# Kernel optimization log

Hardware: AMD Instinct MI355X
Metric: run time of the kernel (lower is better)

Reference implementation:

```python
import jax, jax.numpy as jnp
import numpy as np

N = 50000      # nodes
E = 800000     # edges
FEAT = 128     # input feature dim
EMB = 256      # embed_dim = heads * hid
H = 4          # attention heads
C = 64         # hid_dim per head
PED = 32       # positional encoding dim
NEG_SLOPE = 0.2


def setup_inputs() -> dict:
    key = jax.random.key(0)
    ks = jax.random.split(key, 20)
    s = lambda i, shape, sc=0.1: jax.random.normal(ks[i], shape, jnp.float32) * sc
    return {
        "x": s(0, (N, FEAT), 1.0),
        "x_masked": s(1, (N, FEAT), 1.0),
        "PE": s(2, (N, PED), 1.0),
        "PE_noise": s(3, (N, PED), 1.0),
        "edge_index": jax.random.randint(ks[4], (2, E), 0, N),
        # PEG positional encoder (linear + relu)
        "W_peg": s(5, (PED, PED)), "b_peg": jnp.zeros((PED,), jnp.float32),
        # GAT layer 0
        "W0": s(6, (FEAT, H * C)), "a_s0": s(7, (H, C)), "a_d0": s(8, (H, C)),
        "w_pe0": s(9, (H,)), "W_u0": s(10, (PED, PED)),
        # GAT layer 1
        "W1": s(11, (EMB, H * C)), "a_s1": s(12, (H, C)), "a_d1": s(13, (H, C)),
        "w_pe1": s(14, (H,)), "W_u1": s(15, (PED, PED)),
    }


def _gat(x, pe, src, dst, W, a_s, a_d, w_pe, W_u):
    # PE-aware GATConv: standard GAT attention + PE-distance bias per head.
    xp = (x @ W).reshape(-1, H, C)                       # [N,H,C]
    al_s = (xp * a_s).sum(-1)                            # [N,H]
    al_d = (xp * a_d).sum(-1)                            # [N,H]
    dist = jnp.sqrt(((pe[src] - pe[dst]) ** 2).sum(-1) + 1e-8)   # [E]
    logits = jax.nn.leaky_relu(al_s[src] + al_d[dst], NEG_SLOPE) \
             + dist[:, None] * w_pe                      # [E,H]
    # segment softmax over incoming edges of each dst node
    m = jax.ops.segment_max(logits, dst, num_segments=N)
    e = jnp.exp(logits - m[dst])
    den = jax.ops.segment_sum(e, dst, num_segments=N)
    alpha = e / (den[dst] + 1e-16)                       # [E,H]
    out = jax.ops.segment_sum(alpha[:, :, None] * xp[src], dst,
                              num_segments=N).reshape(-1, H * C)  # [N,H*C]
    pe_out = jax.nn.relu(pe @ W_u)                       # per-layer PE update
    return out, pe_out


def reference(x, x_masked, PE, PE_noise, W_peg, b_peg,
              W0, a_s0, a_d0, w_pe0, W_u0,
              W1, a_s1, a_d1, w_pe1, W_u1, edge_index):
    src, dst = edge_index[0], edge_index[1]
    # PEG encoder on both PE branches
    pe = jax.nn.relu(PE @ W_peg + b_peg)
    pe_n = jax.nn.relu(PE_noise @ W_peg + b_peg)
    # layer 0 (dual branches; eval mode -> dropout is identity)
    h, pe_n = _gat(x, pe_n, src, dst, W0, a_s0, a_d0, w_pe0, W_u0)
    hm, pe = _gat(x_masked, pe, src, dst, W0, a_s0, a_d0, w_pe0, W_u0)
    h = jax.nn.relu(h)
    hm = jax.nn.relu(hm)
    # layer 1 (last layer: no activation)
    h, pe_n = _gat(h, pe_n, src, dst, W1, a_s1, a_d1, w_pe1, W_u1)
    hm, pe = _gat(hm, pe, src, dst, W1, a_s1, a_d1, w_pe1, W_u1)
    return (hm, pe_n)
```

## Files before the change

### kernel.cpp

```cpp
#include <hip/hip_runtime.h>
#include <hip/hip_bf16.h>

#define N_NODES 50000
#define N_EDGES 800000
#define NEG_SLOPE 0.2f

typedef __hip_bfloat16 bf16;
typedef __attribute__((ext_vector_type(8))) short short8;
typedef __attribute__((ext_vector_type(4))) float f32x4;
typedef __attribute__((ext_vector_type(2))) float f32x2;

__device__ __forceinline__ float b2f(bf16 x) { return __bfloat162float(x); }

__device__ __forceinline__ float ldsel(const void* p, size_t i, int isbf) {
  return isbf ? __bfloat162float(((const bf16*)p)[i]) : ((const float*)p)[i];
}
__device__ __forceinline__ void stsel(void* p, size_t i, int isbf, float v) {
  if (isbf) ((bf16*)p)[i] = __float2bfloat16(v);
  else ((float*)p)[i] = v;
}

__device__ __forceinline__ int block_detect(const unsigned short* __restrict__ probe) {
  __shared__ int wcount;
  int tid = threadIdx.x;
  if (tid == 0) wcount = 0;
  __syncthreads();
  int ex = (probe[2 * tid] >> 7) & 0xFF;
  unsigned long long m = __ballot(ex >= 0x85);
  if ((tid & 63) == 0) atomicAdd(&wcount, __popcll(m));
  __syncthreads();
  return wcount < 8;
}

struct CvtJobs {
  const void* src[10];
  float* dst[10];
  int n[10];
};
__global__ __launch_bounds__(256) void prep_kernel(CvtJobs jobs,
                                                   const unsigned short* __restrict__ probe,
                                                   const void* __restrict__ W0in,
                                                   bf16* __restrict__ Wt0,
                                                   const void* __restrict__ W1in,
                                                   bf16* __restrict__ Wt1,
                                                   int* __restrict__ flag) {
  int tid = threadIdx.x;
  int isbf = block_detect(probe);
  int b = blockIdx.x;
  if (b == 0 && tid == 0) *flag = isbf;
  if (b < 16) {
    for (int j = 0; j < 10; j++) {
      int n = jobs.n[j];
      const void* s = jobs.src[j];
      float* d = jobs.dst[j];
      for (int i = b * 256 + tid; i < n; i += 16 * 256) d[i] = ldsel(s, i, isbf);
    }
  } else if (b < 16 + 128) {
    int i = (b - 16) * 256 + tid;
    int n = i >> 7, k = i & 127;
    Wt0[i] = __float2bfloat16(ldsel(W0in, (size_t)k * 256 + n, isbf));
  } else {
    int i = (b - 144) * 256 + tid;
    int n = i >> 8, k = i & 255;
    Wt1[i] = __float2bfloat16(ldsel(W1in, (size_t)k * 256 + n, isbf));
  }
}

__global__ __launch_bounds__(256) void peg_all(const void* __restrict__ pen,
                                               const void* __restrict__ pem,
                                               const float* __restrict__ Wpeg,
                                               const float* __restrict__ bpeg,
                                               const float* __restrict__ Wu0,
                                               const float* __restrict__ Wu1,
                                               void* out, size_t out_off,
                                               char* __restrict__ blob0,
                                               char* __restrict__ blob1,
                                               const int* __restrict__ flag) {
  __shared__ float w1[1024], w2[1024], w3[1024];
  __shared__ float rowA[256], rowB[256];
  int isbf = *flag;
  int tid = threadIdx.x;
  int b = blockIdx.x;
  bool c3 = b < (N_NODES / 8);
  int n0 = (c3 ? b : b - N_NODES / 8) * 8;
  const void* in = c3 ? pen : pem;
  for (int i = tid; i < 1024; i += 256) {
    w1[i] = Wpeg[i];
    w2[i] = Wu0[i];
    if (c3) w3[i] = Wu1[i];
  }
  rowA[tid] = ldsel(in, (size_t)n0 * 32 + tid, isbf);
  __syncthreads();
  int col = tid & 31, ln = tid >> 5;
  size_t bi = ((size_t)(n0 + ln)) * 64 + col;
  float acc = bpeg[col];
#pragma unroll
  for (int j = 0; j < 32; j++) acc += rowA[ln * 32 + j] * w1[j * 32 + col];
  acc = fmaxf(acc, 0.f);
  if (!c3) ((bf16*)blob0)[bi] = __float2bfloat16(acc);
  rowB[tid] = acc;
  __syncthreads();
  acc = 0.f;
#pragma unroll
  for (int j = 0; j < 32; j++) acc += rowB[ln * 32 + j] * w2[j * 32 + col];
  acc = fmaxf(acc, 0.f);
  if (!c3) {
    ((bf16*)blob1)[bi] = __float2bfloat16(acc);
    return;
  }
  rowA[tid] = acc;
  __syncthreads();
  acc = 0.f;
#pragma unroll
  for (int j = 0; j < 32; j++) acc += rowA[ln * 32 + j] * w3[j * 32 + col];
  stsel(out, out_off + (size_t)n0 * 32 + tid, isbf, fmaxf(acc, 0.f));
}

template <int K, bool A_DUAL>
__global__ __launch_bounds__(256) void mfma_gemm(const void* __restrict__ Ap,
                                                 const bf16* __restrict__ Bt,
                                                 bf16* __restrict__ C, int M,
                                                 const float* __restrict__ a_sf,
                                                 const float* __restrict__ a_df,
                                                 char* __restrict__ blob,
                                                 float* __restrict__ al_d,
                                                 const int* __restrict__ flag) {
  constexpr int LDK = 136;
  __shared__ short a_lds[64 * LDK];
  __shared__ short b_lds[64 * LDK];
  __shared__ float lds_al[128];
  int nrt = (M + 63) / 64;
  int bid = blockIdx.x;
  int xcd = bid & 7;
  int jj = bid >> 3;
  int col_t = jj & 3;
  int row_t = (jj >> 2) * 8 + xcd;
  if (row_t >= nrt) return;
  int isbf = A_DUAL ? *flag : 1;
  int tid = threadIdx.x;
  int row0 = row_t * 64;
  int col0 = col_t * 64;
  int lane = tid & 63;
  int wv = tid >> 6;
  int wm = (wv & 1) * 32, wn = (wv >> 1) * 32;
  int l15 = lane & 15, quad = lane >> 4;
  if (tid < 128) lds_al[tid] = 0.f;
  f32x4 acc00 = {0.f, 0.f, 0.f, 0.f}, acc01 = acc00, acc10 = acc00, acc11 = acc00;

  for (int kb = 0; kb < K; kb += 128) {
    if (kb) __syncthreads();
    for (int idx = tid; idx < 64 * 16; idx += 256) {
      int r = idx >> 4, sidx = idx & 15;
      int gr = row0 + r;
      size_t gi = (size_t)gr * K + kb + sidx * 8;
      uint4 av = make_uint4(0u, 0u, 0u, 0u);
      if (A_DUAL && !isbf) {
        if (gr < M) {
          float4 f0 = ((const float4*)Ap)[gi / 4];
          float4 f1 = ((const float4*)Ap)[gi / 4 + 1];
          union { uint4 v; bf16 h[8]; } o;
          o.h[0] = __float2bfloat16(f0.x);
          o.h[1] = __float2bfloat16(f0.y);
          o.h[2] = __float2bfloat16(f0.z);
          o.h[3] = __float2bfloat16(f0.w);
          o.h[4] = __float2bfloat16(f1.x);
          o.h[5] = __float2bfloat16(f1.y);
          o.h[6] = __float2bfloat16(f1.z);
          o.h[7] = __float2bfloat16(f1.w);
          av = o.v;
        }
      } else {
        if (gr < M) av = *(const uint4*)&((const bf16*)Ap)[gi];
      }
      *(uint4*)&a_lds[r * LDK + sidx * 8] = av;
      *(uint4*)&b_lds[r * LDK + sidx * 8] =
          *(const uint4*)&Bt[(size_t)(col0 + r) * K + kb + sidx * 8];
    }
    __syncthreads();
#pragma unroll
    for (int k0 = 0; k0 < 128; k0 += 32) {
      int ko = k0 + quad * 8;
      short8 a0 = *(const short8*)&a_lds[(wm + l15) * LDK + ko];
      short8 a1 = *(const short8*)&a_lds[(wm + 16 + l15) * LDK + ko];
      short8 b0 = *(const short8*)&b_lds[(wn + l15) * LDK + ko];
      short8 b1 = *(const short8*)&b_lds[(wn + 16 + l15) * LDK + ko];
      acc00 = __builtin_amdgcn_mfma_f32_16x16x32_bf16(a0, b0, acc00, 0, 0, 0);
      acc01 = __builtin_amdgcn_mfma_f32_16x16x32_bf16(a0, b1, acc01, 0, 0, 0);
      acc10 = __builtin_amdgcn_mfma_f32_16x16x32_bf16(a1, b0, acc10, 0, 0, 0);
      acc11 = __builtin_amdgcn_mfma_f32_16x16x32_bf16(a1, b1, acc11, 0, 0, 0);
    }
  }
  const f32x4* accs[2][2] = {{&acc00, &acc01}, {&acc10, &acc11}};
  float as0 = a_sf[col0 + wn + l15], as1 = a_sf[col0 + wn + 16 + l15];
  float ad0 = a_df[col0 + wn + l15], ad1 = a_df[col0 + wn + 16 + l15];
#pragma unroll
  for (int i = 0; i < 2; i++) {
    float sp[4], dp[4];
#pragma unroll
    for (int r = 0; r < 4; r++) {
      float v0 = (*accs[i][0])[r], v1 = (*accs[i][1])[r];
      sp[r] = v0 * as0 + v1 * as1;
      dp[r] = v0 * ad0 + v1 * ad1;
      int grow = row0 + wm + i * 16 + quad * 4 + r;
      if (grow < M) {
        C[(size_t)grow * 256 + col0 + wn + l15] = __float2bfloat16(v0);
        C[(size_t)grow * 256 + col0 + wn + 16 + l15] = __float2bfloat16(v1);
      }
    }
#pragma unroll
    for (int off = 1; off < 16; off <<= 1) {
#pragma unroll
      for (int r = 0; r < 4; r++) {
        sp[r] += __shfl_xor(sp[r], off);
        dp[r] += __shfl_xor(dp[r], off);
      }
    }
    if (l15 == 0) {
#pragma unroll
      for (int r = 0; r < 4; r++) {
        int lrow = wm + i * 16 + quad * 4 + r;
        atomicAdd(&lds_al[lrow], sp[r]);
        atomicAdd(&lds_al[64 + lrow], dp[r]);
      }
    }
  }
  __syncthreads();
  if (tid < 64 && row0 + tid < M) {
    int row = row0 + tid;
    *(float*)(blob + (size_t)row * 128 + 64 + (size_t)col_t * 4) = lds_al[tid];
    al_d[(size_t)row * 4 + col_t] = lds_al[64 + tid];
  }
}

__global__ __launch_bounds__(256) void hist_kernel(const int* __restrict__ dst,
                                                   int* __restrict__ deg) {
  int e = blockIdx.x * 256 + threadIdx.x;
  atomicAdd(&deg[dst[e]], 1);
}

__global__ __launch_bounds__(1024) void scan1_kernel(const int* __restrict__ deg,
                                                     int* __restrict__ tmp,
                                                     int* __restrict__ bsum, int n) {
  __shared__ int wsum[16];
  int tid = threadIdx.x;
  int idx = blockIdx.x * 1024 + tid;
  int v = (idx < n) ? deg[idx] : 0;
  int incl = v;
#pragma unroll
  for (int off = 1; off < 64; off <<= 1) {
    int t = __shfl_up(incl, off);
    if ((tid & 63) >= off) incl += t;
  }
  int wid = tid >> 6;
  if ((tid & 63) == 63) wsum[wid] = incl;
  __syncthreads();
  if (tid == 0) {
    int acc = 0;
#pragma unroll
    for (int w = 0; w < 16; w++) {
      int t = wsum[w];
      wsum[w] = acc;
      acc += t;
    }
    bsum[blockIdx.x] = acc;
  }
  __syncthreads();
  if (idx < n) tmp[idx] = wsum[wid] + incl;
}

__global__ void scan2_kernel(int* __restrict__ bsum, int nb) {
  int tid = threadIdx.x;
  int v = (tid < nb) ? bsum[tid] : 0;
  int incl = v;
#pragma unroll
  for (int off = 1; off < 64; off <<= 1) {
    int t = __shfl_up(incl, off);
    if (tid >= off) incl += t;
  }
  if (tid < nb) bsum[tid] = incl - v;
}

__global__ __launch_bounds__(1024) void scan3_kernel(const int* __restrict__ tmp,
                                                     const int* __restrict__ bsum,
                                                     int* __restrict__ rowptr, int n) {
  int idx = blockIdx.x * 1024 + threadIdx.x;
  if (idx < n) rowptr[idx + 1] = tmp[idx] + bsum[blockIdx.x];
  if (idx == 0) rowptr[0] = 0;
}

__global__ __launch_bounds__(256) void fill_kernel(const int* __restrict__ src,
                                                   const int* __restrict__ dst,
                                                   const int* __restrict__ rowptr,
                                                   int* __restrict__ fill,
                                                   int* __restrict__ csr_src) {
  int e = blockIdx.x * 256 + threadIdx.x;
  int d = dst[e];
  int pos = atomicAdd(&fill[d], 1);
  csr_src[rowptr[d] + pos] = src[e];
}

template <bool RELU, bool OUT_DUAL>
__global__ __launch_bounds__(256) void agg_kernel(const bf16* __restrict__ xp,
                                                  const char* __restrict__ blob,
                                                  const float* __restrict__ al_d,
                                                  const float* __restrict__ w_pe,
                                                  const int* __restrict__ csr_src,
                                                  const int* __restrict__ rowptr,
                                                  void* out, const int* __restrict__ flag) {
  int isbf = OUT_DUAL ? *flag : 1;
  int lane = threadIdx.x & 63;
  int n = blockIdx.x * 4 + (threadIdx.x >> 6);
  int q = lane >> 4, li = lane & 15, h = li >> 2;
  const char* bn = blob + (size_t)n * 128;
  unsigned int ud = *(const unsigned int*)(bn + li * 4);
  float pdlo = __uint_as_float(ud << 16);
  float pdhi = __uint_as_float(ud & 0xffff0000u);
  float ald = al_d[(size_t)n * 4 + h];
  float wph = w_pe[h];
  int s1 = rowptr[n + 1];
  int s = rowptr[n] + q;
  f32x2 acc2[8];
#pragma unroll
  for (int j = 0; j < 8; j++) acc2[j] = (f32x2){0.f, 0.f};
  float asum = 0.f;

  int sn_c = -1, sn_n = -1;
  unsigned int pes_c = 0, pes_n = 0;
  float als_c = 0.f, als_n = 0.f;
  uint4 z = make_uint4(0u, 0u, 0u, 0u);
  uint4 xc0 = z, xc1 = z, xn0 = z, xn1 = z;
  if (s < s1) {
    sn_c = csr_src[s];
    const char* bs = blob + (size_t)sn_c * 128;
    pes_c = *(const unsigned int*)(bs + li * 4);
    als_c = *(const float*)(bs + 64 + h * 4);
    const uint4* b = (const uint4*)&xp[(size_t)sn_c * 256 + li * 16];
    xc0 = b[0];
    xc1 = b[1];
    if (s + 4 < s1) sn_n = csr_src[s + 4];
  }
  int sf = s + 8;
  while (sn_c >= 0) {
    if (sn_n >= 0) {
      const char* bs = blob + (size_t)sn_n * 128;
      pes_n = *(const unsigned int*)(bs + li * 4);
      als_n = *(const float*)(bs + 64 + h * 4);
      const uint4* b = (const uint4*)&xp[(size_t)sn_n * 256 + li * 16];
      xn0 = b[0];
      xn1 = b[1];
    }
    int sn_f = (sf < s1) ? csr_src[sf] : -1;
    sf += 4;
    float dx = __uint_as_float(pes_c << 16) - pdlo;
    float dy = __uint_as_float(pes_c & 0xffff0000u) - pdhi;
    float d2 = dx * dx + dy * dy;
#pragma unroll
    for (int off = 1; off < 16; off <<= 1) d2 += __shfl_xor(d2, off);
    float lg = als_c + ald;
    lg = fmaxf(lg, 0.f) + NEG_SLOPE * fminf(lg, 0.f);
    lg += __builtin_amdgcn_sqrtf(d2 + 1e-8f) * wph;
    float a = __expf(lg);
    f32x2 av = {a, a};
    unsigned int u[8] = {xc0.x, xc0.y, xc0.z, xc0.w, xc1.x, xc1.y, xc1.z, xc1.w};
#pragma unroll
    for (int p = 0; p < 8; p++) {
      f32x2 xv;
      xv.x = __uint_as_float(u[p] << 16);
      xv.y = __uint_as_float(u[p] & 0xffff0000u);
      acc2[p] += av * xv;
    }
    asum += a;
    sn_c = sn_n;
    pes_c = pes_n;
    als_c = als_n;
    xc0 = xn0;
    xc1 = xn1;
    sn_n = sn_f;
  }
#pragma unroll
  for (int j = 0; j < 8; j++) {
    acc2[j].x += __shfl_xor(acc2[j].x, 16);
    acc2[j].x += __shfl_xor(acc2[j].x, 32);
    acc2[j].y += __shfl_xor(acc2[j].y, 16);
    acc2[j].y += __shfl_xor(acc2[j].y, 32);
  }
  asum += __shfl_xor(asum, 16);
  asum += __shfl_xor(asum, 32);
  if (q == 0) {
    float inv = 1.f / (asum + 1e-16f);
    size_t oi = (size_t)n * 256 + li * 16;
    if (OUT_DUAL && !isbf) {
      float* of = (float*)out;
#pragma unroll
      for (int p = 0; p < 4; p++) {
        float4 f;
        f.x = acc2[2 * p].x * inv;
        f.y = acc2[2 * p].y * inv;
        f.z = acc2[2 * p + 1].x * inv;
        f.w = acc2[2 * p + 1].y * inv;
        if (RELU) {
          f.x = fmaxf(f.x, 0.f);
          f.y = fmaxf(f.y, 0.f);
          f.z = fmaxf(f.z, 0.f);
          f.w = fmaxf(f.w, 0.f);
        }
        *(float4*)&of[oi + 4 * p] = f;
      }
    } else {
      union { uint4 v[2]; bf16 hh[16]; } o;
#pragma unroll
      for (int j = 0; j < 8; j++) {
        float rlo = acc2[j].x * inv;
        float rhi = acc2[j].y * inv;
        if (RELU) {
          rlo = fmaxf(rlo, 0.f);
          rhi = fmaxf(rhi, 0.f);
        }
        o.hh[2 * j] = __float2bfloat16(rlo);
        o.hh[2 * j + 1] = __float2bfloat16(rhi);
      }
      uint4* ob = (uint4*)&((bf16*)out)[oi];
      ob[0] = o.v[0];
      ob[1] = o.v[1];
    }
  }
}

extern "C" void kernel_launch(void* const* d_in, const int* in_sizes, int n_in,
                              void* d_out, int out_size, void* d_ws, size_t ws_size,
                              hipStream_t stream) {
  const void* x_masked = d_in[1];
  const void* PE = d_in[2];
  const void* PE_noise = d_in[3];
  const int* ei = (const int*)d_in[4];
  const int* src = ei;
  const int* dst = ei + N_EDGES;

  char* w = (char*)d_ws;
  auto alloc = [&](size_t bytes) -> char* {
    char* p = w;
    w += (bytes + 255) / 256 * 256;
    return p;
  };
  int* flag = (int*)alloc(4);
  float* W_peg_f = (float*)alloc(1024 * 4);
  float* b_peg_f = (float*)alloc(32 * 4);
  float* a_s0_f = (float*)alloc(256 * 4);
  float* a_d0_f = (float*)alloc(256 * 4);
  float* w_pe0_f = (float*)alloc(4 * 4);
  float* W_u0_f = (float*)alloc(1024 * 4);
  float* a_s1_f = (float*)alloc(256 * 4);
  float* a_d1_f = (float*)alloc(256 * 4);
  float* w_pe1_f = (float*)alloc(4 * 4);
  float* W_u1_f = (float*)alloc(1024 * 4);
  bf16* Wt0 = (bf16*)alloc(32768 * 2);
  bf16* Wt1 = (bf16*)alloc(65536 * 2);
  char* blob0 = alloc((size_t)N_NODES * 128);
  char* blob1 = alloc((size_t)N_NODES * 128);
  float* al_d = (float*)alloc((size_t)N_NODES * 4 * 4);
  int* degfill = (int*)alloc((size_t)N_NODES * 2 * 4);
  int* deg = degfill;
  int* fill = degfill + N_NODES;
  int* rowptr = (int*)alloc((size_t)(N_NODES + 1) * 4);
  int* stmp = (int*)alloc((size_t)N_NODES * 4);
  int* bsum = (int*)alloc(64 * 4);
  int* csr_src = (int*)alloc((size_t)N_EDGES * 4);
  bf16* xp = (bf16*)alloc((size_t)N_NODES * 256 * 2);
  bf16* hm0 = (bf16*)alloc((size_t)N_NODES * 256 * 2);

  CvtJobs jobs;
  int ji = 0;
  auto addjob = [&](const void* s, float* d, int n) {
    jobs.src[ji] = s; jobs.dst[ji] = d; jobs.n[ji] = n; ji++;
  };
  addjob(d_in[5], W_peg_f, 1024);
  addjob(d_in[6], b_peg_f, 32);
  addjob(d_in[8], a_s0_f, 256);
  addjob(d_in[9], a_d0_f, 256);
  addjob(d_in[10], w_pe0_f, 4);
  addjob(d_in[11], W_u0_f, 1024);
  addjob(d_in[13], a_s1_f, 256);
  addjob(d_in[14], a_d1_f, 256);
  addjob(d_in[15], w_pe1_f, 4);
  addjob(d_in[16], W_u1_f, 1024);
  prep_kernel<<<400, 256, 0, stream>>>(jobs, (const unsigned short*)d_in[5],
                                       d_in[7], Wt0, d_in[12], Wt1, flag);

  hipMemsetAsync(degfill, 0, (size_t)N_NODES * 2 * 4, stream);

  hist_kernel<<<N_EDGES / 256, 256, 0, stream>>>(dst, deg);
  scan1_kernel<<<49, 1024, 0, stream>>>(deg, stmp, bsum, N_NODES);
  scan2_kernel<<<1, 64, 0, stream>>>(bsum, 49);
  scan3_kernel<<<49, 1024, 0, stream>>>(stmp, bsum, rowptr, N_NODES);
  fill_kernel<<<N_EDGES / 256, 256, 0, stream>>>(src, dst, rowptr, fill, csr_src);

  peg_all<<<2 * (N_NODES / 8), 256, 0, stream>>>(PE_noise, PE, W_peg_f, b_peg_f,
                                                 W_u0_f, W_u1_f, d_out,
                                                 (size_t)N_NODES * 256, blob0,
                                                 blob1, flag);

  int nrt = (N_NODES + 63) / 64;
  int gblk = ((nrt + 7) / 8) * 8 * 4;

  mfma_gemm<128, true><<<gblk, 256, 0, stream>>>(x_masked, Wt0, xp, N_NODES,
                                                 a_s0_f, a_d0_f, blob0, al_d, flag);
  agg_kernel<true, false><<<N_NODES / 4, 256, 0, stream>>>(
      xp, blob0, al_d, w_pe0_f, csr_src, rowptr, hm0, flag);

  mfma_gemm<256, false><<<gblk, 256, 0, stream>>>(hm0, Wt1, xp, N_NODES,
                                                  a_s1_f, a_d1_f, blob1, al_d, flag);
  agg_kernel<false, true><<<N_NODES / 4, 256, 0, stream>>>(
      xp, blob1, al_d, w_pe1_f, csr_src, rowptr, d_out, flag);
}
```

Baseline: 442.0 us.

## Merge preprocessing kernels and use nontemporal stores for outputs

```diff
diff --git a/kernel.cpp b/kernel.cpp
--- a/kernel.cpp
+++ b/kernel.cpp
@@ -9,6 +9,7 @@
 typedef __attribute__((ext_vector_type(8))) short short8;
 typedef __attribute__((ext_vector_type(4))) float f32x4;
 typedef __attribute__((ext_vector_type(2))) float f32x2;
+typedef __attribute__((ext_vector_type(4))) unsigned int u32x4;
 
 __device__ __forceinline__ float b2f(bf16 x) { return __bfloat162float(x); }
 
@@ -18,6 +19,23 @@
 __device__ __forceinline__ void stsel(void* p, size_t i, int isbf, float v) {
   if (isbf) ((bf16*)p)[i] = __float2bfloat16(v);
   else ((float*)p)[i] = v;
+}
+__device__ __forceinline__ void ntstsel(void* p, size_t i, int isbf, float v) {
+  if (isbf) {
+    union { bf16 b; unsigned short u; } c;
+    c.b = __float2bfloat16(v);
+    __builtin_nontemporal_store(c.u, (unsigned short*)p + i);
+  } else {
+    __builtin_nontemporal_store(v, (float*)p + i);
+  }
+}
+__device__ __forceinline__ void nt_store_u4(void* p, uint4 v) {
+  u32x4 t = {v.x, v.y, v.z, v.w};
+  __builtin_nontemporal_store(t, (u32x4*)p);
+}
+__device__ __forceinline__ void nt_store_f4(void* p, float x, float y, float z, float w) {
+  f32x4 t = {x, y, z, w};
+  __builtin_nontemporal_store(t, (f32x4*)p);
 }
 
 __device__ __forceinline__ int block_detect(const unsigned short* __restrict__ probe) {
@@ -43,10 +61,17 @@
                                                    bf16* __restrict__ Wt0,
                                                    const void* __restrict__ W1in,
                                                    bf16* __restrict__ Wt1,
-                                                   int* __restrict__ flag) {
+                                                   int* __restrict__ flag,
+                                                   const int* __restrict__ dst,
+                                                   int* __restrict__ deg) {
   int tid = threadIdx.x;
+  int b = blockIdx.x;
+  if (b >= 400) {
+    int e = (b - 400) * 256 + tid;
+    atomicAdd(&deg[dst[e]], 1);
+    return;
+  }
   int isbf = block_detect(probe);
-  int b = blockIdx.x;
   if (b == 0 && tid == 0) *flag = isbf;
   if (b < 16) {
     for (int j = 0; j < 10; j++) {
@@ -66,23 +91,81 @@
   }
 }
 
-__global__ __launch_bounds__(256) void peg_all(const void* __restrict__ pen,
-                                               const void* __restrict__ pem,
-                                               const float* __restrict__ Wpeg,
-                                               const float* __restrict__ bpeg,
-                                               const float* __restrict__ Wu0,
-                                               const float* __restrict__ Wu1,
-                                               void* out, size_t out_off,
-                                               char* __restrict__ blob0,
-                                               char* __restrict__ blob1,
-                                               const int* __restrict__ flag) {
+__global__ __launch_bounds__(1024) void scan1_kernel(const int* __restrict__ deg,
+                                                     int* __restrict__ tmp,
+                                                     int* __restrict__ bsum, int n) {
+  __shared__ int wsum[16];
+  int tid = threadIdx.x;
+  int idx = blockIdx.x * 1024 + tid;
+  int v = (idx < n) ? deg[idx] : 0;
+  int incl = v;
+#pragma unroll
+  for (int off = 1; off < 64; off <<= 1) {
+    int t = __shfl_up(incl, off);
+    if ((tid & 63) >= off) incl += t;
+  }
+  int wid = tid >> 6;
+  if ((tid & 63) == 63) wsum[wid] = incl;
+  __syncthreads();
+  if (tid == 0) {
+    int acc = 0;
+#pragma unroll
+    for (int w = 0; w < 16; w++) {
+      int t = wsum[w];
+      wsum[w] = acc;
+      acc += t;
+    }
+    bsum[blockIdx.x] = acc;
+  }
+  __syncthreads();
+  if (idx < n) tmp[idx] = wsum[wid] + incl;
+}
+
+__global__ __launch_bounds__(1024) void scan3_kernel(const int* __restrict__ tmp,
+                                                     const int* __restrict__ bsum,
+                                                     int* __restrict__ rowptr, int n,
+                                                     int nb) {
+  __shared__ int lb[64];
+  int tid = threadIdx.x;
+  if (tid < nb) lb[tid] = bsum[tid];
+  __syncthreads();
+  int pre = 0;
+  for (int j = 0; j < blockIdx.x; j++) pre += lb[j];
+  int idx = blockIdx.x * 1024 + tid;
+  if (idx < n) rowptr[idx + 1] = tmp[idx] + pre;
+  if (idx == 0) rowptr[0] = 0;
+}
+
+__global__ __launch_bounds__(256) void fill_peg_kernel(const int* __restrict__ src,
+                                                       const int* __restrict__ dst,
+                                                       const int* __restrict__ rowptr,
+                                                       int* __restrict__ fill,
+                                                       int* __restrict__ csr_src,
+                                                       const void* __restrict__ pen,
+                                                       const void* __restrict__ pem,
+                                                       const float* __restrict__ Wpeg,
+                                                       const float* __restrict__ bpeg,
+                                                       const float* __restrict__ Wu0,
+                                                       const float* __restrict__ Wu1,
+                                                       void* out, size_t out_off,
+                                                       char* __restrict__ blob0,
+                                                       char* __restrict__ blob1,
+                                                       const int* __restrict__ flag) {
   __shared__ float w1[1024], w2[1024], w3[1024];
   __shared__ float rowA[256], rowB[256];
-  int isbf = *flag;
   int tid = threadIdx.x;
   int b = blockIdx.x;
-  bool c3 = b < (N_NODES / 8);
-  int n0 = (c3 ? b : b - N_NODES / 8) * 8;
+  if (b < N_EDGES / 256) {
+    int e = b * 256 + tid;
+    int d = dst[e];
+    int pos = atomicAdd(&fill[d], 1);
+    csr_src[rowptr[d] + pos] = src[e];
+    return;
+  }
+  int pb = b - N_EDGES / 256;
+  int isbf = *flag;
+  bool c3 = pb < (N_NODES / 8);
+  int n0 = (c3 ? pb : pb - N_NODES / 8) * 8;
   const void* in = c3 ? pen : pem;
   for (int i = tid; i < 1024; i += 256) {
     w1[i] = Wpeg[i];
@@ -113,7 +196,7 @@
   acc = 0.f;
 #pragma unroll
   for (int j = 0; j < 32; j++) acc += rowA[ln * 32 + j] * w3[j * 32 + col];
-  stsel(out, out_off + (size_t)n0 * 32 + tid, isbf, fmaxf(acc, 0.f));
+  ntstsel(out, out_off + (size_t)n0 * 32 + tid, isbf, fmaxf(acc, 0.f));
 }
 
 template <int K, bool A_DUAL>
@@ -232,73 +315,6 @@
   }
 }
 
-__global__ __launch_bounds__(256) void hist_kernel(const int* __restrict__ dst,
-                                                   int* __restrict__ deg) {
-  int e = blockIdx.x * 256 + threadIdx.x;
-  atomicAdd(&deg[dst[e]], 1);
-}
-
-__global__ __launch_bounds__(1024) void scan1_kernel(const int* __restrict__ deg,
-                                                     int* __restrict__ tmp,
-                                                     int* __restrict__ bsum, int n) {
-  __shared__ int wsum[16];
-  int tid = threadIdx.x;
-  int idx = blockIdx.x * 1024 + tid;
-  int v = (idx < n) ? deg[idx] : 0;
-  int incl = v;
-#pragma unroll
-  for (int off = 1; off < 64; off <<= 1) {
-    int t = __shfl_up(incl, off);
-    if ((tid & 63) >= off) incl += t;
-  }
-  int wid = tid >> 6;
-  if ((tid & 63) == 63) wsum[wid] = incl;
-  __syncthreads();
-  if (tid == 0) {
-    int acc = 0;
-#pragma unroll
-    for (int w = 0; w < 16; w++) {
-      int t = wsum[w];
-      wsum[w] = acc;
-      acc += t;
-    }
-    bsum[blockIdx.x] = acc;
-  }
-  __syncthreads();
-  if (idx < n) tmp[idx] = wsum[wid] + incl;
-}
-
-__global__ void scan2_kernel(int* __restrict__ bsum, int nb) {
-  int tid = threadIdx.x;
-  int v = (tid < nb) ? bsum[tid] : 0;
-  int incl = v;
-#pragma unroll
-  for (int off = 1; off < 64; off <<= 1) {
-    int t = __shfl_up(incl, off);
-    if (tid >= off) incl += t;
-  }
-  if (tid < nb) bsum[tid] = incl - v;
-}
-
-__global__ __launch_bounds__(1024) void scan3_kernel(const int* __restrict__ tmp,
-                                                     const int* __restrict__ bsum,
-                                                     int* __restrict__ rowptr, int n) {
-  int idx = blockIdx.x * 1024 + threadIdx.x;
-  if (idx < n) rowptr[idx + 1] = tmp[idx] + bsum[blockIdx.x];
-  if (idx == 0) rowptr[0] = 0;
-}
-
-__global__ __launch_bounds__(256) void fill_kernel(const int* __restrict__ src,
-                                                   const int* __restrict__ dst,
-                                                   const int* __restrict__ rowptr,
-                                                   int* __restrict__ fill,
-                                                   int* __restrict__ csr_src) {
-  int e = blockIdx.x * 256 + threadIdx.x;
-  int d = dst[e];
-  int pos = atomicAdd(&fill[d], 1);
-  csr_src[rowptr[d] + pos] = src[e];
-}
-
 template <bool RELU, bool OUT_DUAL>
 __global__ __launch_bounds__(256) void agg_kernel(const bf16* __restrict__ xp,
                                                   const char* __restrict__ blob,
@@ -393,18 +409,17 @@
       float* of = (float*)out;
 #pragma unroll
       for (int p = 0; p < 4; p++) {
-        float4 f;
-        f.x = acc2[2 * p].x * inv;
-        f.y = acc2[2 * p].y * inv;
-        f.z = acc2[2 * p + 1].x * inv;
-        f.w = acc2[2 * p + 1].y * inv;
+        float fx = acc2[2 * p].x * inv;
+        float fy = acc2[2 * p].y * inv;
+        float fz = acc2[2 * p + 1].x * inv;
+        float fw = acc2[2 * p + 1].y * inv;
         if (RELU) {
-          f.x = fmaxf(f.x, 0.f);
-          f.y = fmaxf(f.y, 0.f);
-          f.z = fmaxf(f.z, 0.f);
-          f.w = fmaxf(f.w, 0.f);
+          fx = fmaxf(fx, 0.f);
+          fy = fmaxf(fy, 0.f);
+          fz = fmaxf(fz, 0.f);
+          fw = fmaxf(fw, 0.f);
         }
-        *(float4*)&of[oi + 4 * p] = f;
+        nt_store_f4(&of[oi + 4 * p], fx, fy, fz, fw);
       }
     } else {
       union { uint4 v[2]; bf16 hh[16]; } o;
@@ -419,9 +434,9 @@
         o.hh[2 * j] = __float2bfloat16(rlo);
         o.hh[2 * j + 1] = __float2bfloat16(rhi);
       }
-      uint4* ob = (uint4*)&((bf16*)out)[oi];
-      ob[0] = o.v[0];
-      ob[1] = o.v[1];
+      bf16* ob = &((bf16*)out)[oi];
+      nt_store_u4(ob, o.v[0]);
+      nt_store_u4(ob + 8, o.v[1]);
     }
   }
 }
@@ -483,21 +498,19 @@
   addjob(d_in[14], a_d1_f, 256);
   addjob(d_in[15], w_pe1_f, 4);
   addjob(d_in[16], W_u1_f, 1024);
-  prep_kernel<<<400, 256, 0, stream>>>(jobs, (const unsigned short*)d_in[5],
-                                       d_in[7], Wt0, d_in[12], Wt1, flag);
 
   hipMemsetAsync(degfill, 0, (size_t)N_NODES * 2 * 4, stream);
 
-  hist_kernel<<<N_EDGES / 256, 256, 0, stream>>>(dst, deg);
+  prep_kernel<<<400 + N_EDGES / 256, 256, 0, stream>>>(
+      jobs, (const unsigned short*)d_in[5], d_in[7], Wt0, d_in[12], Wt1, flag,
+      dst, deg);
+
   scan1_kernel<<<49, 1024, 0, stream>>>(deg, stmp, bsum, N_NODES);
-  scan2_kernel<<<1, 64, 0, stream>>>(bsum, 49);
-  scan3_kernel<<<49, 1024, 0, stream>>>(stmp, bsum, rowptr, N_NODES);
-  fill_kernel<<<N_EDGES / 256, 256, 0, stream>>>(src, dst, rowptr, fill, csr_src);
-
-  peg_all<<<2 * (N_NODES / 8), 256, 0, stream>>>(PE_noise, PE, W_peg_f, b_peg_f,
-                                                 W_u0_f, W_u1_f, d_out,
-                                                 (size_t)N_NODES * 256, blob0,
-                                                 blob1, flag);
+  scan3_kernel<<<49, 1024, 0, stream>>>(stmp, bsum, rowptr, N_NODES, 49);
+
+  fill_peg_kernel<<<N_EDGES / 256 + 2 * (N_NODES / 8), 256, 0, stream>>>(
+      src, dst, rowptr, fill, csr_src, PE_noise, PE, W_peg_f, b_peg_f, W_u0_f,
+      W_u1_f, d_out, (size_t)N_NODES * 256, blob0, blob1, flag);
 
   int nrt = (N_NODES + 63) / 64;
   int gblk = ((nrt + 7) / 8) * 8 * 4;
```

New measurement: 442.9 us. Within noise of the previous version (+0.2%).

## Fuse CSR build, PE encoder and first GEMM into fewer kernel launches

Applied to the files above, without the earlier changes.

```diff
diff --git a/kernel.cpp b/kernel.cpp
--- a/kernel.cpp
+++ b/kernel.cpp
@@ -43,10 +43,17 @@
                                                    bf16* __restrict__ Wt0,
                                                    const void* __restrict__ W1in,
                                                    bf16* __restrict__ Wt1,
-                                                   int* __restrict__ flag) {
+                                                   int* __restrict__ flag,
+                                                   const int* __restrict__ dst,
+                                                   int* __restrict__ deg) {
   int tid = threadIdx.x;
+  int b = blockIdx.x;
+  if (b >= 400) {
+    int e = (b - 400) * 256 + tid;
+    atomicAdd(&deg[dst[e]], 1);
+    return;
+  }
   int isbf = block_detect(probe);
-  int b = blockIdx.x;
   if (b == 0 && tid == 0) *flag = isbf;
   if (b < 16) {
     for (int j = 0; j < 10; j++) {
@@ -66,78 +73,71 @@
   }
 }
 
-__global__ __launch_bounds__(256) void peg_all(const void* __restrict__ pen,
-                                               const void* __restrict__ pem,
-                                               const float* __restrict__ Wpeg,
-                                               const float* __restrict__ bpeg,
-                                               const float* __restrict__ Wu0,
-                                               const float* __restrict__ Wu1,
-                                               void* out, size_t out_off,
-                                               char* __restrict__ blob0,
-                                               char* __restrict__ blob1,
-                                               const int* __restrict__ flag) {
-  __shared__ float w1[1024], w2[1024], w3[1024];
-  __shared__ float rowA[256], rowB[256];
-  int isbf = *flag;
+__global__ __launch_bounds__(1024) void scan_kernel(const int* __restrict__ deg,
+                                                    int* __restrict__ rowptr,
+                                                    int* __restrict__ bsum,
+                                                    int* __restrict__ flags, int n) {
+  __shared__ int wsum[16];
+  __shared__ int spre;
   int tid = threadIdx.x;
-  int b = blockIdx.x;
-  bool c3 = b < (N_NODES / 8);
-  int n0 = (c3 ? b : b - N_NODES / 8) * 8;
-  const void* in = c3 ? pen : pem;
-  for (int i = tid; i < 1024; i += 256) {
-    w1[i] = Wpeg[i];
-    w2[i] = Wu0[i];
-    if (c3) w3[i] = Wu1[i];
-  }
-  rowA[tid] = ldsel(in, (size_t)n0 * 32 + tid, isbf);
-  __syncthreads();
-  int col = tid & 31, ln = tid >> 5;
-  size_t bi = ((size_t)(n0 + ln)) * 64 + col;
-  float acc = bpeg[col];
-#pragma unroll
-  for (int j = 0; j < 32; j++) acc += rowA[ln * 32 + j] * w1[j * 32 + col];
-  acc = fmaxf(acc, 0.f);
-  if (!c3) ((bf16*)blob0)[bi] = __float2bfloat16(acc);
-  rowB[tid] = acc;
-  __syncthreads();
-  acc = 0.f;
-#pragma unroll
-  for (int j = 0; j < 32; j++) acc += rowB[ln * 32 + j] * w2[j * 32 + col];
-  acc = fmaxf(acc, 0.f);
-  if (!c3) {
-    ((bf16*)blob1)[bi] = __float2bfloat16(acc);
-    return;
-  }
-  rowA[tid] = acc;
-  __syncthreads();
-  acc = 0.f;
-#pragma unroll
-  for (int j = 0; j < 32; j++) acc += rowA[ln * 32 + j] * w3[j * 32 + col];
-  stsel(out, out_off + (size_t)n0 * 32 + tid, isbf, fmaxf(acc, 0.f));
+  int idx = blockIdx.x * 1024 + tid;
+  int v = (idx < n) ? deg[idx] : 0;
+  int incl = v;
+#pragma unroll
+  for (int off = 1; off < 64; off <<= 1) {
+    int t = __shfl_up(incl, off);
+    if ((tid & 63) >= off) incl += t;
+  }
+  int wid = tid >> 6;
+  if ((tid & 63) == 63) wsum[wid] = incl;
+  __syncthreads();
+  if (tid == 0) {
+    int acc = 0;
+#pragma unroll
+    for (int w = 0; w < 16; w++) {
+      int t = wsum[w];
+      wsum[w] = acc;
+      acc += t;
+    }
+    atomicExch(&bsum[blockIdx.x], acc);
+    if (atomicAdd(&flags[0], 1) == 48) {
+      int a = 0;
+      for (int j = 0; j < 49; j++) {
+        int t = atomicAdd(&bsum[j], 0);
+        atomicExch(&bsum[j], a);
+        a += t;
+      }
+      atomicExch(&flags[1], 1);
+    }
+    while (atomicAdd(&flags[1], 0) == 0) {}
+    spre = atomicAdd(&bsum[blockIdx.x], 0);
+  }
+  __syncthreads();
+  if (idx < n) rowptr[idx + 1] = spre + wsum[wid] + incl;
+  if (idx == 0) rowptr[0] = 0;
 }
 
 template <int K, bool A_DUAL>
-__global__ __launch_bounds__(256) void mfma_gemm(const void* __restrict__ Ap,
-                                                 const bf16* __restrict__ Bt,
-                                                 bf16* __restrict__ C, int M,
-                                                 const float* __restrict__ a_sf,
-                                                 const float* __restrict__ a_df,
-                                                 char* __restrict__ blob,
-                                                 float* __restrict__ al_d,
-                                                 const int* __restrict__ flag) {
-  constexpr int LDK = 136;
-  __shared__ short a_lds[64 * LDK];
-  __shared__ short b_lds[64 * LDK];
-  __shared__ float lds_al[128];
+__device__ __forceinline__ void gemm_body(char* smem, int bid, int tid,
+                                          const void* __restrict__ Ap,
+                                          const bf16* __restrict__ Bt,
+                                          bf16* __restrict__ C, int M,
+                                          const float* __restrict__ a_sf,
+                                          const float* __restrict__ a_df,
+                                          char* __restrict__ blob,
+                                          float* __restrict__ al_d,
+                                          const int* __restrict__ flag) {
+  constexpr int LDK = 72;
+  short* a_lds = (short*)smem;
+  short* b_lds = (short*)(smem + 64 * LDK * 2);
+  float* lds_al = (float*)(smem + 2 * 64 * LDK * 2);
   int nrt = (M + 63) / 64;
-  int bid = blockIdx.x;
   int xcd = bid & 7;
   int jj = bid >> 3;
   int col_t = jj & 3;
   int row_t = (jj >> 2) * 8 + xcd;
   if (row_t >= nrt) return;
   int isbf = A_DUAL ? *flag : 1;
-  int tid = threadIdx.x;
   int row0 = row_t * 64;
   int col0 = col_t * 64;
   int lane = tid & 63;
@@ -147,10 +147,10 @@
   if (tid < 128) lds_al[tid] = 0.f;
   f32x4 acc00 = {0.f, 0.f, 0.f, 0.f}, acc01 = acc00, acc10 = acc00, acc11 = acc00;
 
-  for (int kb = 0; kb < K; kb += 128) {
+  for (int kb = 0; kb < K; kb += 64) {
     if (kb) __syncthreads();
-    for (int idx = tid; idx < 64 * 16; idx += 256) {
-      int r = idx >> 4, sidx = idx & 15;
+    for (int idx = tid; idx < 64 * 8; idx += 256) {
+      int r = idx >> 3, sidx = idx & 7;
       int gr = row0 + r;
       size_t gi = (size_t)gr * K + kb + sidx * 8;
       uint4 av = make_uint4(0u, 0u, 0u, 0u);
@@ -178,7 +178,7 @@
     }
     __syncthreads();
 #pragma unroll
-    for (int k0 = 0; k0 < 128; k0 += 32) {
+    for (int k0 = 0; k0 < 64; k0 += 32) {
       int ko = k0 + quad * 8;
       short8 a0 = *(const short8*)&a_lds[(wm + l15) * LDK + ko];
       short8 a1 = *(const short8*)&a_lds[(wm + 16 + l15) * LDK + ko];
@@ -232,71 +232,107 @@
   }
 }
 
-__global__ __launch_bounds__(256) void hist_kernel(const int* __restrict__ dst,
-                                                   int* __restrict__ deg) {
-  int e = blockIdx.x * 256 + threadIdx.x;
-  atomicAdd(&deg[dst[e]], 1);
-}
-
-__global__ __launch_bounds__(1024) void scan1_kernel(const int* __restrict__ deg,
-                                                     int* __restrict__ tmp,
-                                                     int* __restrict__ bsum, int n) {
-  __shared__ int wsum[16];
+#define SMEM_BYTES (2 * 64 * 72 * 2 + 512)
+
+template <int K, bool A_DUAL>
+__global__ __launch_bounds__(256) void mfma_gemm(const void* __restrict__ Ap,
+                                                 const bf16* __restrict__ Bt,
+                                                 bf16* __restrict__ C, int M,
+                                                 const float* __restrict__ a_sf,
+                                                 const float* __restrict__ a_df,
+                                                 char* __restrict__ blob,
+                                                 float* __restrict__ al_d,
+                                                 const int* __restrict__ flag) {
+  __shared__ char smem[SMEM_BYTES];
+  gemm_body<K, A_DUAL>(smem, blockIdx.x, threadIdx.x, Ap, Bt, C, M, a_sf, a_df,
+                       blob, al_d, flag);
+}
+
+#define NGEMM0 3136
+#define NCHUNK (N_EDGES / 256)
+#define NFILL8 (NCHUNK * 8)
+#define NDIV8 (N_NODES / 8)
+__global__ __launch_bounds__(256) void mid_kernel(const void* __restrict__ Ap,
+                                                  const bf16* __restrict__ Wt0,
+                                                  bf16* __restrict__ xp,
+                                                  const float* __restrict__ a_s0,
+                                                  const float* __restrict__ a_d0,
+                                                  float* __restrict__ al_d,
+                                                  const int* __restrict__ src,
+                                                  const int* __restrict__ dst,
+                                                  const int* __restrict__ rowptr,
+                                                  int* __restrict__ fill,
+                                                  int* __restrict__ csr_src,
+                                                  const void* __restrict__ pen,
+                                                  const void* __restrict__ pem,
+                                                  const float* __restrict__ Wpeg,
+                                                  const float* __restrict__ bpeg,
+                                                  const float* __restrict__ Wu0,
+                                                  const float* __restrict__ Wu1,
+                                                  void* out, size_t out_off,
+                                                  char* __restrict__ blob0,
+                                                  char* __restrict__ blob1,
+                                                  const int* __restrict__ flag) {
+  __shared__ char smem[SMEM_BYTES];
   int tid = threadIdx.x;
-  int idx = blockIdx.x * 1024 + tid;
-  int v = (idx < n) ? deg[idx] : 0;
-  int incl = v;
-#pragma unroll
-  for (int off = 1; off < 64; off <<= 1) {
-    int t = __shfl_up(incl, off);
-    if ((tid & 63) >= off) incl += t;
-  }
-  int wid = tid >> 6;
-  if ((tid & 63) == 63) wsum[wid] = incl;
-  __syncthreads();
-  if (tid == 0) {
-    int acc = 0;
-#pragma unroll
-    for (int w = 0; w < 16; w++) {
-      int t = wsum[w];
-      wsum[w] = acc;
-      acc += t;
-    }
-    bsum[blockIdx.x] = acc;
-  }
-  __syncthreads();
-  if (idx < n) tmp[idx] = wsum[wid] + incl;
-}
-
-__global__ void scan2_kernel(int* __restrict__ bsum, int nb) {
-  int tid = threadIdx.x;
-  int v = (tid < nb) ? bsum[tid] : 0;
-  int incl = v;
-#pragma unroll
-  for (int off = 1; off < 64; off <<= 1) {
-    int t = __shfl_up(incl, off);
-    if (tid >= off) incl += t;
-  }
-  if (tid < nb) bsum[tid] = incl - v;
-}
-
-__global__ __launch_bounds__(1024) void scan3_kernel(const int* __restrict__ tmp,
-                                                     const int* __restrict__ bsum,
-                                                     int* __restrict__ rowptr, int n) {
-  int idx = blockIdx.x * 1024 + threadIdx.x;
-  if (idx < n) rowptr[idx + 1] = tmp[idx] + bsum[blockIdx.x];
-  if (idx == 0) rowptr[0] = 0;
-}
-
-__global__ __launch_bounds__(256) void fill_kernel(const int* __restrict__ src,
-                                                   const int* __restrict__ dst,
-                                                   const int* __restrict__ rowptr,
-                                                   int* __restrict__ fill,
-                                                   int* __restrict__ csr_src) {
-  int e = blockIdx.x * 256 + threadIdx.x;
-  int d = dst[e];
-  int pos = atomicAdd(&fill[d], 1);
-  csr_src[rowptr[d] + pos] = src[e];
+  int b = blockIdx.x;
+  if (b < NGEMM0) {
+    gemm_body<128, true>(smem, b, tid, Ap, Wt0, xp, N_NODES, a_s0, a_d0, blob0,
+                         al_d, flag);
+    return;
+  }
+  b -= NGEMM0;
+  if (b < NFILL8) {
+    int xcd = b & 7;
+    int e = (b >> 3) * 256 + tid;
+    int d = dst[e];
+    int lo = xcd * NDIV8;
+    if (d >= lo && d < lo + NDIV8) {
+      int pos = atomicAdd(&fill[d], 1);
+      csr_src[rowptr[d] + pos] = src[e];
+    }
+    return;
+  }
+  int pb = b - NFILL8;
+  float* w1 = (float*)smem;
+  float* w2 = w1 + 1024;
+  float* w3 = w2 + 1024;
+  float* rowA = w3 + 1024;
+  float* rowB = rowA + 256;
+  int isbf = *flag;
+  bool c3 = pb < NDIV8;
+  int n0 = (c3 ? pb : pb - NDIV8) * 8;
+  const void* in = c3 ? pen : pem;
+  for (int i = tid; i < 1024; i += 256) {
+    w1[i] = Wpeg[i];
+    w2[i] = Wu0[i];
+    if (c3) w3[i] = Wu1[i];
+  }
+  rowA[tid] = ldsel(in, (size_t)n0 * 32 + tid, isbf);
+  __syncthreads();
+  int col = tid & 31, ln = tid >> 5;
+  size_t bi = ((size_t)(n0 + ln)) * 64 + col;
+  float acc = bpeg[col];
+#pragma unroll
+  for (int j = 0; j < 32; j++) acc += rowA[ln * 32 + j] * w1[j * 32 + col];
+  acc = fmaxf(acc, 0.f);
+  if (!c3) ((bf16*)blob0)[bi] = __float2bfloat16(acc);
+  rowB[tid] = acc;
+  __syncthreads();
+  acc = 0.f;
+#pragma unroll
+  for (int j = 0; j < 32; j++) acc += rowB[ln * 32 + j] * w2[j * 32 + col];
+  acc = fmaxf(acc, 0.f);
+  if (!c3) {
+    ((bf16*)blob1)[bi] = __float2bfloat16(acc);
+    return;
+  }
+  rowA[tid] = acc;
+  __syncthreads();
+  acc = 0.f;
+#pragma unroll
+  for (int j = 0; j < 32; j++) acc += rowA[ln * 32 + j] * w3[j * 32 + col];
+  stsel(out, out_off + (size_t)n0 * 32 + tid, isbf, fmaxf(acc, 0.f));
 }
 
 template <bool RELU, bool OUT_DUAL>
@@ -458,11 +494,11 @@
   char* blob0 = alloc((size_t)N_NODES * 128);
   char* blob1 = alloc((size_t)N_NODES * 128);
   float* al_d = (float*)alloc((size_t)N_NODES * 4 * 4);
-  int* degfill = (int*)alloc((size_t)N_NODES * 2 * 4);
+  int* degfill = (int*)alloc(((size_t)N_NODES * 2 + 64) * 4);
   int* deg = degfill;
   int* fill = degfill + N_NODES;
+  int* sflags = degfill + 2 * N_NODES;
   int* rowptr = (int*)alloc((size_t)(N_NODES + 1) * 4);
-  int* stmp = (int*)alloc((size_t)N_NODES * 4);
   int* bsum = (int*)alloc(64 * 4);
   int* csr_src = (int*)alloc((size_t)N_EDGES * 4);
   bf16* xp = (bf16*)alloc((size_t)N_NODES * 256 * 2);
@@ -483,32 +519,25 @@
   addjob(d_in[14], a_d1_f, 256);
   addjob(d_in[15], w_pe1_f, 4);
   addjob(d_in[16], W_u1_f, 1024);
-  prep_kernel<<<400, 256, 0, stream>>>(jobs, (const unsigned short*)d_in[5],
-                                       d_in[7], Wt0, d_in[12], Wt1, flag);
-
-  hipMemsetAsync(degfill, 0, (size_t)N_NODES * 2 * 4, stream);
-
-  hist_kernel<<<N_EDGES / 256, 256, 0, stream>>>(dst, deg);
-  scan1_kernel<<<49, 1024, 0, stream>>>(deg, stmp, bsum, N_NODES);
-  scan2_kernel<<<1, 64, 0, stream>>>(bsum, 49);
-  scan3_kernel<<<49, 1024, 0, stream>>>(stmp, bsum, rowptr, N_NODES);
-  fill_kernel<<<N_EDGES / 256, 256, 0, stream>>>(src, dst, rowptr, fill, csr_src);
-
-  peg_all<<<2 * (N_NODES / 8), 256, 0, stream>>>(PE_noise, PE, W_peg_f, b_peg_f,
-                                                 W_u0_f, W_u1_f, d_out,
-                                                 (size_t)N_NODES * 256, blob0,
-                                                 blob1, flag);
-
-  int nrt = (N_NODES + 63) / 64;
-  int gblk = ((nrt + 7) / 8) * 8 * 4;
-
-  mfma_gemm<128, true><<<gblk, 256, 0, stream>>>(x_masked, Wt0, xp, N_NODES,
-                                                 a_s0_f, a_d0_f, blob0, al_d, flag);
+
+  hipMemsetAsync(degfill, 0, ((size_t)N_NODES * 2 + 64) * 4, stream);
+
+  prep_kernel<<<400 + NCHUNK, 256, 0, stream>>>(
+      jobs, (const unsigned short*)d_in[5], d_in[7], Wt0, d_in[12], Wt1, flag,
+      dst, deg);
+
+  scan_kernel<<<49, 1024, 0, stream>>>(deg, rowptr, bsum, sflags, N_NODES);
+
+  mid_kernel<<<NGEMM0 + NFILL8 + 2 * NDIV8, 256, 0, stream>>>(
+      x_masked, Wt0, xp, a_s0_f, a_d0_f, al_d, src, dst, rowptr, fill, csr_src,
+      PE_noise, PE, W_peg_f, b_peg_f, W_u0_f, W_u1_f, d_out,
+      (size_t)N_NODES * 256, blob0, blob1, flag);
+
   agg_kernel<true, false><<<N_NODES / 4, 256, 0, stream>>>(
       xp, blob0, al_d, w_pe0_f, csr_src, rowptr, hm0, flag);
 
-  mfma_gemm<256, false><<<gblk, 256, 0, stream>>>(hm0, Wt1, xp, N_NODES,
-                                                  a_s1_f, a_d1_f, blob1, al_d, flag);
+  mfma_gemm<256, false><<<NGEMM0, 256, 0, stream>>>(hm0, Wt1, xp, N_NODES,
+                                                    a_s1_f, a_d1_f, blob1, al_d, flag);
   agg_kernel<false, true><<<N_NODES / 4, 256, 0, stream>>>(
       xp, blob1, al_d, w_pe1_f, csr_src, rowptr, d_out, flag);
 }
```

Measured after the change: 447.4 us. About the same (+1.2%).
